# Kernel tuning notes

Measured on AMD Instinct MI355X. Metric: run time of the kernel, lower is better.

Reference implementation:

```python
import jax, jax.numpy as jnp
import numpy as np

DIM, H, KV, HD = 2048, 32, 8, 64
NREP = H // KV
EPS = 1e-6
NEG = -1e30


def _rope(x, cos, sin):
    # x: [B,S,h,HD], cos/sin: [S,HD//2]
    xr, xi = x[..., 0::2], x[..., 1::2]
    c = cos[None, :, None, :]
    s = sin[None, :, None, :]
    out = jnp.stack([xr * c - xi * s, xr * s + xi * c], axis=-1)
    return out.reshape(x.shape)


def _rmsnorm(x, w):
    xf = x.astype(jnp.float32)
    inv = jax.lax.rsqrt(jnp.mean(xf * xf, axis=-1, keepdims=True) + EPS)
    return (xf * inv * w).astype(x.dtype)


def setup_inputs() -> dict:
    key = jax.random.key(0)
    ks = jax.random.split(key, 9)
    B, S = 1, 2048
    x = jax.random.normal(ks[0], (B, S, DIM), jnp.float32)
    cos = jax.random.uniform(ks[1], (S, HD // 2), jnp.float32)
    sin = jax.random.uniform(ks[2], (S, HD // 2), jnp.float32)
    sc = 1.0 / np.sqrt(DIM)
    wq = jax.random.normal(ks[3], (DIM, DIM), jnp.float32) * sc
    wk = jax.random.normal(ks[4], (KV * HD, DIM), jnp.float32) * sc
    wv = jax.random.normal(ks[5], (KV * HD, DIM), jnp.float32) * sc
    wo = jax.random.normal(ks[6], (DIM, DIM), jnp.float32) * sc
    wg = jax.random.normal(ks[7], (DIM, DIM), jnp.float32) * sc
    qn = jnp.ones((HD,), jnp.float32)
    kn = jnp.ones((HD,), jnp.float32)
    return {"x": x, "cos": cos, "sin": sin, "wq": wq, "wk": wk, "wv": wv,
            "wo": wo, "wg": wg, "qn": qn, "kn": kn}


def reference(x, cos, sin, wq, wk, wv, wo, wg, qn, kn):
    B, S, _ = x.shape
    q = (x @ wq.T).reshape(B, S, H, HD)
    k = (x @ wk.T).reshape(B, S, KV, HD)
    v = (x @ wv.T).reshape(B, S, KV, HD)
    q = _rope(q, cos, sin)
    k = _rope(k, cos, sin)
    q = _rmsnorm(q, qn)
    k = _rmsnorm(k, kn)
    # GQA without materializing repeat_kv: head h = g*NREP + r uses kv head g
    qg = q.reshape(B, S, KV, NREP, HD)
    scale = 1.0 / np.sqrt(HD)
    scores = jnp.einsum('bqgrd,bkgd->bgrqk', qg, k) * scale  # [B,KV,NREP,S,S]
    causal = jnp.tril(jnp.ones((S, S), bool))
    scores = jnp.where(causal, scores, NEG)
    attn = jax.nn.softmax(scores, axis=-1)
    o = jnp.einsum('bgrqk,bkgd->bqgrd', attn, v).reshape(B, S, DIM)
    o = o * jax.nn.sigmoid(x @ wg.T)
    return o @ wo.T
```

## Files before the change

kernel.cpp:

```cpp
#include <hip/hip_runtime.h>
#include <stdint.h>

typedef unsigned short u16;
typedef unsigned int u32;
typedef __bf16 bf16x8 __attribute__((ext_vector_type(8)));
typedef __bf16 bf16x2 __attribute__((ext_vector_type(2)));
typedef float f32x4 __attribute__((ext_vector_type(4)));

__device__ __forceinline__ float bf2f(u16 u) {
  union { unsigned int i; float f; } v; v.i = ((unsigned int)u) << 16; return v.f;
}
__device__ __forceinline__ u16 f2bf(float f) {
  union { float f; unsigned int i; } v; v.f = f;
  unsigned int r = v.i + 0x7fffu + ((v.i >> 16) & 1u);
  return (u16)(r >> 16);
}
__device__ __forceinline__ void ld16(const void* g, void* l) {
  __builtin_amdgcn_global_load_lds(
      (const __attribute__((address_space(1))) unsigned int*)g,
      (__attribute__((address_space(3))) unsigned int*)l, 16, 0, 0);
}

__global__ __launch_bounds__(256) void k_cast(
    const float* __restrict__ s0, u16* __restrict__ d0,
    const float* __restrict__ s1, u16* __restrict__ d1,
    const float* __restrict__ s2, u16* __restrict__ d2,
    const float* __restrict__ s3, u16* __restrict__ d3,
    const float* __restrict__ s4, u16* __restrict__ d4,
    const float* __restrict__ s5, u16* __restrict__ d5)
{
  int b = blockIdx.x;
  const float* s; u16* d;
  if (b < 4096)       { s = s0; d = d0; }
  else if (b < 8192)  { s = s1; d = d1; b -= 4096; }
  else if (b < 9216)  { s = s2; d = d2; b -= 8192; }
  else if (b < 10240) { s = s3; d = d3; b -= 9216; }
  else if (b < 14336) { s = s4; d = d4; b -= 10240; }
  else                { s = s5; d = d5; b -= 14336; }
  const int i = (b * 256 + threadIdx.x) * 4;
  const float4 v = *(const float4*)(s + i);
  ushort4 o;
  o.x = f2bf(v.x); o.y = f2bf(v.y); o.z = f2bf(v.z); o.w = f2bf(v.w);
  *(ushort4*)(d + i) = o;
}

template <typename OT>
__device__ __forceinline__ void gemm_body(
    const u16* __restrict__ A, int lda,
    const u16* __restrict__ B, int ldb,
    OT* __restrict__ C, int ldc, int K,
    u16* As, u16* Bs)
{
  const int tid = threadIdx.x;
  const int wave = tid >> 6, lane = tid & 63;
  const int wrow = (wave >> 1) * 64, wcol = (wave & 1) * 64;
  const int fr = lane & 15, kg = lane >> 4;
  const int srl = lane >> 3;
  const int scg = (lane & 7) ^ srl;

  f32x4 acc[4][4];
  const f32x4 z = {0.f, 0.f, 0.f, 0.f};
  for (int i = 0; i < 4; i++) for (int j = 0; j < 4; j++) acc[i][j] = z;

  const u16* Ag = A + (size_t)(wave * 8 + srl) * lda + scg * 8;
  const u16* Bg = B + (size_t)(wave * 8 + srl) * ldb + scg * 8;
  u16* Asw = As + wave * 8 * 64;
  u16* Bsw = Bs + wave * 8 * 64;
  const int sxr = fr & 7;

  for (int k0 = 0; k0 < K; k0 += 64) {
    for (int i = 0; i < 4; i++) {
      ld16(Ag + k0 + (size_t)(i * 32) * lda, Asw + i * 32 * 64);
      ld16(Bg + k0 + (size_t)(i * 32) * ldb, Bsw + i * 32 * 64);
    }
    __syncthreads();
    bf16x8 af[4][2], bfr[4][2];
    for (int i = 0; i < 4; i++)
      for (int h = 0; h < 2; h++) {
        af[i][h]  = *(const bf16x8*)&As[(wrow + i * 16 + fr) * 64 + (((h * 4 + kg) ^ sxr)) * 8];
        bfr[i][h] = *(const bf16x8*)&Bs[(wcol + i * 16 + fr) * 64 + (((h * 4 + kg) ^ sxr)) * 8];
      }
    for (int h = 0; h < 2; h++)
      for (int mi = 0; mi < 4; mi++)
        for (int ni = 0; ni < 4; ni++)
          acc[mi][ni] = __builtin_amdgcn_mfma_f32_16x16x32_bf16(af[mi][h], bfr[ni][h], acc[mi][ni], 0, 0, 0);
    __syncthreads();
  }
  const int er = kg * 4, ec = fr;
  for (int mi = 0; mi < 4; mi++)
    for (int ni = 0; ni < 4; ni++)
      for (int r = 0; r < 4; r++) {
        const float v = acc[mi][ni][r];
        OT* p = C + (size_t)(wrow + mi * 16 + er + r) * ldc + wcol + ni * 16 + ec;
        if constexpr (sizeof(OT) == 2) *p = (OT)f2bf(v); else *p = (OT)v;
      }
}

__global__ __launch_bounds__(256) void k_gemm_qkvg(
    const u16* __restrict__ x, const u16* __restrict__ wq, const u16* __restrict__ wk,
    const u16* __restrict__ wv, const u16* __restrict__ wg, u16* __restrict__ out)
{
  __shared__ __align__(16) u16 As[128 * 64];
  __shared__ __align__(16) u16 Bs[128 * 64];
  const int m0 = blockIdx.x * 128;
  const int c0 = blockIdx.y * 128;
  const u16* B; int br;
  if (c0 < 2048)      { B = wq; br = c0; }
  else if (c0 < 2560) { B = wk; br = c0 - 2048; }
  else if (c0 < 3072) { B = wv; br = c0 - 2560; }
  else                { B = wg; br = c0 - 3072; }
  gemm_body<u16>(x + (size_t)m0 * 2048, 2048, B + (size_t)br * 2048, 2048,
                 out + (size_t)m0 * 5120 + c0, 5120, 2048, As, Bs);
}

__global__ __launch_bounds__(256) void k_gemm_out(
    const u16* __restrict__ a, const u16* __restrict__ wo, float* __restrict__ out)
{
  __shared__ __align__(16) u16 As[128 * 64];
  __shared__ __align__(16) u16 Bs[128 * 64];
  const int m0 = blockIdx.x * 128;
  const int c0 = blockIdx.y * 128;
  gemm_body<float>(a + (size_t)m0 * 2048, 2048, wo + (size_t)c0 * 2048, 2048,
                   out + (size_t)m0 * 2048 + c0, 2048, 2048, As, Bs);
}

__global__ __launch_bounds__(256) void k_prep(
    u16* __restrict__ qkvg, const float* __restrict__ cosp, const float* __restrict__ sinp,
    const float* __restrict__ qn, const float* __restrict__ kn, u16* __restrict__ vt)
{
  __shared__ u16 Ls[64 * 72];
  if (blockIdx.x < 10240) {
    const int wid = (blockIdx.x * 256 + threadIdx.x) >> 6;
    const int lane = threadIdx.x & 63;
    const int s = wid / 20, hp = wid - s * 20;
    const int h = hp * 2 + (lane >> 5);
    const int j = lane & 31;
    u16* base; const float* wn;
    if (h < 32) { base = qkvg + (size_t)s * 5120 + h * 64;                wn = qn; }
    else        { base = qkvg + (size_t)s * 5120 + 2048 + (h - 32) * 64; wn = kn; }
    const unsigned int u = *(const unsigned int*)(base + 2 * j);
    const float xr = bf2f((u16)(u & 0xffffu)), xi = bf2f((u16)(u >> 16));
    const float c = cosp[s * 32 + j], sn = sinp[s * 32 + j];
    const float o0 = xr * c - xi * sn;
    const float o1 = xr * sn + xi * c;
    float ss = o0 * o0 + o1 * o1;
    for (int m = 1; m <= 16; m <<= 1) ss += __shfl_xor(ss, m, 64);
    const float inv = rsqrtf(ss * (1.0f / 64.0f) + 1e-6f);
    const u16 r0 = f2bf(o0 * inv * wn[2 * j]);
    const u16 r1 = f2bf(o1 * inv * wn[2 * j + 1]);
    *(unsigned int*)(base + 2 * j) = (unsigned int)r0 | ((unsigned int)r1 << 16);
  } else {
    const int bb = blockIdx.x - 10240;
    const int s0 = (bb & 31) * 64, g0 = (bb >> 5) * 64;
    const int tid = threadIdx.x;
    const int lr = tid >> 4, lc = (tid & 15) * 4;
    for (int p = 0; p < 4; p++) {
      const int r = p * 16 + lr;
      *(ushort4*)&Ls[r * 72 + lc] = *(const ushort4*)&qkvg[(size_t)(s0 + r) * 5120 + 2560 + g0 + lc];
    }
    __syncthreads();
    for (int p = 0; p < 4; p++) {
      const int r = p * 16 + lr;
      ushort4 o;
      o.x = Ls[(lc + 0) * 72 + r];
      o.y = Ls[(lc + 1) * 72 + r];
      o.z = Ls[(lc + 2) * 72 + r];
      o.w = Ls[(lc + 3) * 72 + r];
      *(ushort4*)&vt[(size_t)(g0 + r) * 2048 + s0 + lc] = o;
    }
  }
}

__global__ __launch_bounds__(256) void k_attn_part(
    const u16* __restrict__ qkvg, const u16* __restrict__ vt,
    u16* __restrict__ part, float* __restrict__ ml)
{
  __shared__ __align__(16) u16 Ks[128 * 64];
  __shared__ __align__(16) u16 Vs[64 * 128];
  u16* Ps = Ks;
  const int c = blockIdx.x, h = blockIdx.y, g = h >> 2;
  int qt, ci;
  if (c < 8)       { qt = c;                 ci = 0; }
  else if (c < 24) { qt = 8 + ((c - 8) >> 1);  ci = (c - 8) & 1; }
  else if (c < 48) { qt = 16 + (c - 24) / 3;   ci = (c - 24) % 3; }
  else             { qt = 24 + ((c - 48) >> 2); ci = (c - 48) & 3; }
  const int kb0 = ci * 512;
  const int kend = min(kb0 + 512, (qt + 1) * 64);
  const int q0 = qt * 64;
  const int tid = threadIdx.x, wave = tid >> 6, lane = tid & 63;
  const int fr = lane & 15, kg = lane >> 4, fq = kg * 8;
  const int sx = fr & 7;

  {
    const u16* Qg = qkvg + (size_t)(q0 + wave * 16 + (lane >> 3)) * 5120 + h * 64 + (lane & 7) * 8;
    ld16(Qg, Ks + wave * 1024);
    ld16(Qg + (size_t)8 * 5120, Ks + wave * 1024 + 512);
  }
  __syncthreads();
  const bf16x8 aq0 = *(const bf16x8*)&Ks[(wave * 16 + fr) * 64 + fq];
  const bf16x8 aq1 = *(const bf16x8*)&Ks[(wave * 16 + fr) * 64 + 32 + fq];
  __syncthreads();

  f32x4 o[4];
  const f32x4 z = {0.f, 0.f, 0.f, 0.f};
  for (int i = 0; i < 4; i++) o[i] = z;
  float L = 0.f;
  const int qrow = q0 + wave * 16 + fr;
  const int prow = wave * 16 + fr;

  const int krl = wave * 8 + (lane >> 3);
  const int kcg = (lane & 7) ^ (krl & 7);
  const int vrl = wave * 4 + kg;
  const int vcg = fr ^ (vrl & 7);

  for (int kb = kb0; kb < kend; kb += 128) {
    {
      const u16* Kg = qkvg + (size_t)(kb + krl) * 5120 + 2048 + g * 64 + kcg * 8;
      for (int i = 0; i < 4; i++)
        ld16(Kg + (size_t)(i * 32) * 5120, Ks + (i * 32 + wave * 8) * 64);
    }
    {
      const u16* Vg = vt + (size_t)(g * 64 + vrl) * 2048 + kb + vcg * 8;
      for (int i = 0; i < 4; i++)
        ld16(Vg + (size_t)(i * 16) * 2048, Vs + (i * 16 + wave * 4) * 128);
    }
    __syncthreads();

    f32x4 sc[8];
    for (int i = 0; i < 8; i++) sc[i] = z;
    __builtin_amdgcn_s_setprio(1);
    for (int ni = 0; ni < 8; ni++) {
      const bf16x8 bk0 = *(const bf16x8*)&Ks[(ni * 16 + fr) * 64 + ((kg ^ sx)) * 8];
      const bf16x8 bk1 = *(const bf16x8*)&Ks[(ni * 16 + fr) * 64 + (((kg + 4) ^ sx)) * 8];
      sc[ni] = __builtin_amdgcn_mfma_f32_16x16x32_bf16(bk0, aq0, sc[ni], 0, 0, 0);
      sc[ni] = __builtin_amdgcn_mfma_f32_16x16x32_bf16(bk1, aq1, sc[ni], 0, 0, 0);
    }
    __builtin_amdgcn_s_setprio(0);
    __syncthreads();

    u32* Ps32 = (u32*)Ps;
    const int pb32 = prow * 64;
    if (kb + 127 > q0 + wave * 16) {
      for (int ni = 0; ni < 8; ni++) {
        const int dlim = qrow - (kb + ni * 16 + kg * 4);
        float p0 = exp2f(fmaf(sc[ni][0], 0.18033688f, -11.5415603f));
        float p1 = exp2f(fmaf(sc[ni][1], 0.18033688f, -11.5415603f));
        float p2 = exp2f(fmaf(sc[ni][2], 0.18033688f, -11.5415603f));
        float p3 = exp2f(fmaf(sc[ni][3], 0.18033688f, -11.5415603f));
        p0 = (0 <= dlim) ? p0 : 0.f;
        p1 = (1 <= dlim) ? p1 : 0.f;
        p2 = (2 <= dlim) ? p2 : 0.f;
        p3 = (3 <= dlim) ? p3 : 0.f;
        L += (p0 + p1) + (p2 + p3);
        bf16x2 w0, w1;
        w0[0] = (__bf16)p0; w0[1] = (__bf16)p1;
        w1[0] = (__bf16)p2; w1[1] = (__bf16)p3;
        const int a = pb32 + ((2 * ni + (kg >> 1)) ^ sx) * 4 + (kg & 1) * 2;
        *(bf16x2*)&Ps32[a]     = w0;
        *(bf16x2*)&Ps32[a + 1] = w1;
      }
    } else {
      for (int ni = 0; ni < 8; ni++) {
        float p0 = exp2f(fmaf(sc[ni][0], 0.18033688f, -11.5415603f));
        float p1 = exp2f(fmaf(sc[ni][1], 0.18033688f, -11.5415603f));
        float p2 = exp2f(fmaf(sc[ni][2], 0.18033688f, -11.5415603f));
        float p3 = exp2f(fmaf(sc[ni][3], 0.18033688f, -11.5415603f));
        L += (p0 + p1) + (p2 + p3);
        bf16x2 w0, w1;
        w0[0] = (__bf16)p0; w0[1] = (__bf16)p1;
        w1[0] = (__bf16)p2; w1[1] = (__bf16)p3;
        const int a = pb32 + ((2 * ni + (kg >> 1)) ^ sx) * 4 + (kg & 1) * 2;
        *(bf16x2*)&Ps32[a]     = w0;
        *(bf16x2*)&Ps32[a + 1] = w1;
      }
    }

    __builtin_amdgcn_s_setprio(1);
    for (int k0 = 0; k0 < 128; k0 += 32) {
      const bf16x8 ap = *(const bf16x8*)&Ps[prow * 128 + ((((k0 >> 3) + kg)) ^ sx) * 8];
      for (int ni = 0; ni < 4; ni++) {
        const bf16x8 bv = *(const bf16x8*)&Vs[(ni * 16 + fr) * 128 + (((k0 >> 3) + kg) ^ sx) * 8];
        o[ni] = __builtin_amdgcn_mfma_f32_16x16x32_bf16(ap, bv, o[ni], 0, 0, 0);
      }
    }
    __builtin_amdgcn_s_setprio(0);
    __syncthreads();
  }

  L += __shfl_xor(L, 16, 64);
  L += __shfl_xor(L, 32, 64);
  const int pbase = (h * 80 + c) * 4096;
  for (int ni = 0; ni < 4; ni++)
    for (int r = 0; r < 4; r++)
      part[pbase + (wave * 16 + kg * 4 + r) * 64 + ni * 16 + fr] = f2bf(o[ni][r]);
  if (lane < 16) ml[(h * 80 + c) * 64 + wave * 16 + fr] = L;
}

__global__ __launch_bounds__(256) void k_attn_comb(
    const u16* __restrict__ part, const float* __restrict__ ml,
    const u16* __restrict__ qkvg, u16* __restrict__ aout)
{
  const int qt = blockIdx.x, h = blockIdx.y;
  const int w = threadIdx.x >> 6, lane = threadIdx.x & 63;
  int cb, nch;
  if (qt < 8)       { cb = qt;               nch = 1; }
  else if (qt < 16) { cb = 8 + 2 * (qt - 8);  nch = 2; }
  else if (qt < 24) { cb = 24 + 3 * (qt - 16); nch = 3; }
  else              { cb = 48 + 4 * (qt - 24); nch = 4; }
  for (int r = 0; r < 16; r++) {
    const int rl = w * 16 + r;
    const int row = qt * 64 + rl;
    float L = 0.f, o = 0.f;
    for (int cc = 0; cc < nch; cc++) {
      L += ml[(h * 80 + cb + cc) * 64 + rl];
      o += bf2f(part[(h * 80 + cb + cc) * 4096 + rl * 64 + lane]);
    }
    const float gv = bf2f(qkvg[(size_t)row * 5120 + 3072 + h * 64 + lane]);
    const float sig = 1.0f / (1.0f + __expf(-gv));
    aout[(size_t)row * 2048 + h * 64 + lane] = f2bf(o / L * sig);
  }
}

extern "C" void kernel_launch(void* const* d_in, const int* in_sizes, int n_in,
                              void* d_out, int out_size, void* d_ws, size_t ws_size,
                              hipStream_t stream)
{
  const float* x  = (const float*)d_in[0];
  const float* cs = (const float*)d_in[1];
  const float* sn = (const float*)d_in[2];
  const float* wq = (const float*)d_in[3];
  const float* wk = (const float*)d_in[4];
  const float* wv = (const float*)d_in[5];
  const float* wo = (const float*)d_in[6];
  const float* wg = (const float*)d_in[7];
  const float* qn = (const float*)d_in[8];
  const float* kn = (const float*)d_in[9];
  float* out = (float*)d_out;

  u16* xb   = (u16*)d_ws;
  u16* wqb  = xb  + (size_t)4194304;
  u16* wkb  = wqb + (size_t)4194304;
  u16* wvb  = wkb + (size_t)1048576;
  u16* wgb  = wvb + (size_t)1048576;
  u16* wob  = wgb + (size_t)4194304;
  u16* qkvg = wob + (size_t)4194304;
  u16* vt   = qkvg + (size_t)2048 * 5120;
  u16* aws  = vt   + (size_t)512 * 2048;

  u16*   part = xb;
  float* ml   = (float*)(xb + (size_t)32 * 80 * 4096);

  k_cast<<<dim3(18432), 256, 0, stream>>>(x, xb, wq, wqb, wk, wkb, wv, wvb, wo, wob, wg, wgb);
  k_gemm_qkvg<<<dim3(16, 40), 256, 0, stream>>>(xb, wqb, wkb, wvb, wgb, qkvg);
  k_prep<<<dim3(10240 + 256), 256, 0, stream>>>(qkvg, cs, sn, qn, kn, vt);
  k_attn_part<<<dim3(80, 32), 256, 0, stream>>>(qkvg, vt, part, ml);
  k_attn_comb<<<dim3(32, 32), 256, 0, stream>>>(part, ml, qkvg, aws);
  k_gemm_out<<<dim3(16, 16), 256, 0, stream>>>(aws, wob, out);
}
```

Baseline: 291.5 us.

## Rewrite QKVG projection GEMM as 256x256 double-buffered pipelined kernel

Replaces the 128x128 single-buffered QKVG projection GEMM with a 256x256-tile, 512-thread kernel. It double-buffers LDS and interleaves global-to-LDS async loads for the next K-steps with MFMA phases, using setprio and fine-grained barriers. The goal is to hide memory latency and raise arithmetic intensity per block. The cost is 128 KB of LDS per block and only 160 blocks, which may underfill the device's compute units and limit occupancy.

Measured after the change: 307.0 us. 5.3% more time.

```diff
diff --git a/kernel.cpp b/kernel.cpp
--- a/kernel.cpp
+++ b/kernel.cpp
@@ -44,6 +44,157 @@
   *(ushort4*)(d + i) = o;
 }
 
+__device__ __forceinline__ void stage256(const u16* __restrict__ gb, int k0, int half,
+                                         u16* __restrict__ Lb, int wave)
+{
+  const u16* src = gb + (size_t)(half * 128) * 2048 + k0;
+  u16* dst = Lb + (half * 128 + wave * 8) * 64;
+  ld16(src, dst);
+  ld16(src + (size_t)64 * 2048, dst + 64 * 64);
+}
+
+__global__ __launch_bounds__(512, 2) void k_gemm_qkvg(
+    const u16* __restrict__ x, const u16* __restrict__ wq, const u16* __restrict__ wk,
+    const u16* __restrict__ wv, const u16* __restrict__ wg, u16* __restrict__ out)
+{
+  __shared__ __align__(16) u16 As[2][256 * 64];
+  __shared__ __align__(16) u16 Bs[2][256 * 64];
+  const int mt = blockIdx.x & 7, nt = blockIdx.x >> 3;
+  const int m0 = mt * 256, c0 = nt * 256;
+  const u16* Bm; int br;
+  if (c0 < 2048)      { Bm = wq; br = c0; }
+  else if (c0 < 2560) { Bm = wk; br = c0 - 2048; }
+  else if (c0 < 3072) { Bm = wv; br = c0 - 2560; }
+  else                { Bm = wg; br = c0 - 3072; }
+
+  const int tid = threadIdx.x, wave = tid >> 6, lane = tid & 63;
+  const int wr = wave >> 2, wc = wave & 3;
+  const int fr = lane & 15, kg = lane >> 4, sx = fr & 7;
+  const int srl = lane >> 3, scg = (lane & 7) ^ srl;
+
+  const u16* Ag = x  + (size_t)(m0 + wave * 8 + srl) * 2048 + scg * 8;
+  const u16* Bg = Bm + (size_t)(br + wave * 8 + srl) * 2048 + scg * 8;
+
+  stage256(Ag,  0, 0, As[0], wave);
+  stage256(Ag,  0, 1, As[0], wave);
+  stage256(Bg,  0, 0, Bs[0], wave);
+  stage256(Bg,  0, 1, Bs[0], wave);
+  stage256(Bg, 64, 0, Bs[1], wave);
+  stage256(Bg, 64, 1, Bs[1], wave);
+  stage256(Ag, 64, 0, As[1], wave);
+  asm volatile("s_waitcnt vmcnt(6)" ::: "memory");
+  __builtin_amdgcn_s_barrier();
+
+  f32x4 acc[8][4];
+  const f32x4 z = {0.f, 0.f, 0.f, 0.f};
+#pragma unroll
+  for (int i = 0; i < 8; i++)
+#pragma unroll
+    for (int j = 0; j < 4; j++) acc[i][j] = z;
+
+  for (int t = 0; t < 32; ++t) {
+    const int cur = t & 1;
+    const u16* Ac = As[cur];
+    const u16* Bc = Bs[cur];
+    u16* An = As[cur ^ 1];
+    u16* A2 = As[cur];  u16* B2 = Bs[cur];
+    const int k1 = (t + 1 < 32 ? t + 1 : 31) * 64;
+    const int k2 = (t + 2 < 32 ? t + 2 : 31) * 64;
+
+    bf16x8 bfr[4][2], af0[2][2];
+#pragma unroll
+    for (int ni = 0; ni < 4; ni++)
+#pragma unroll
+      for (int h = 0; h < 2; h++)
+        bfr[ni][h] = *(const bf16x8*)&Bc[(wc * 64 + ni * 16 + fr) * 64 + (((h * 4 + kg) ^ sx)) * 8];
+#pragma unroll
+    for (int m2 = 0; m2 < 2; m2++)
+#pragma unroll
+      for (int h = 0; h < 2; h++)
+        af0[m2][h] = *(const bf16x8*)&Ac[(wr * 128 + m2 * 16 + fr) * 64 + (((h * 4 + kg) ^ sx)) * 8];
+    stage256(Ag, k1, 1, An, wave);
+    __builtin_amdgcn_s_barrier();
+    asm volatile("s_waitcnt lgkmcnt(0)" ::: "memory");
+    __builtin_amdgcn_s_setprio(1);
+#pragma unroll
+    for (int h = 0; h < 2; h++)
+#pragma unroll
+      for (int m2 = 0; m2 < 2; m2++)
+#pragma unroll
+        for (int ni = 0; ni < 4; ni++)
+          acc[m2][ni] = __builtin_amdgcn_mfma_f32_16x16x32_bf16(af0[m2][h], bfr[ni][h], acc[m2][ni], 0, 0, 0);
+    __builtin_amdgcn_s_setprio(0);
+    __builtin_amdgcn_s_barrier();
+
+    bf16x8 af1[2][2];
+#pragma unroll
+    for (int m2 = 0; m2 < 2; m2++)
+#pragma unroll
+      for (int h = 0; h < 2; h++)
+        af1[m2][h] = *(const bf16x8*)&Ac[(wr * 128 + (2 + m2) * 16 + fr) * 64 + (((h * 4 + kg) ^ sx)) * 8];
+    stage256(Bg, k2, 0, B2, wave);
+    __builtin_amdgcn_s_barrier();
+    asm volatile("s_waitcnt lgkmcnt(0)" ::: "memory");
+    __builtin_amdgcn_s_setprio(1);
+#pragma unroll
+    for (int h = 0; h < 2; h++)
+#pragma unroll
+      for (int m2 = 0; m2 < 2; m2++)
+#pragma unroll
+        for (int ni = 0; ni < 4; ni++)
+          acc[2 + m2][ni] = __builtin_amdgcn_mfma_f32_16x16x32_bf16(af1[m2][h], bfr[ni][h], acc[2 + m2][ni], 0, 0, 0);
+    __builtin_amdgcn_s_setprio(0);
+    __builtin_amdgcn_s_barrier();
+
+    bf16x8 af2[2][2], af3[2][2];
+#pragma unroll
+    for (int m2 = 0; m2 < 2; m2++)
+#pragma unroll
+      for (int h = 0; h < 2; h++) {
+        af2[m2][h] = *(const bf16x8*)&Ac[(wr * 128 + (4 + m2) * 16 + fr) * 64 + (((h * 4 + kg) ^ sx)) * 8];
+        af3[m2][h] = *(const bf16x8*)&Ac[(wr * 128 + (6 + m2) * 16 + fr) * 64 + (((h * 4 + kg) ^ sx)) * 8];
+      }
+    stage256(Bg, k2, 1, B2, wave);
+    __builtin_amdgcn_s_barrier();
+    asm volatile("s_waitcnt lgkmcnt(0)" ::: "memory");
+    __builtin_amdgcn_s_setprio(1);
+#pragma unroll
+    for (int h = 0; h < 2; h++)
+#pragma unroll
+      for (int m2 = 0; m2 < 2; m2++)
+#pragma unroll
+        for (int ni = 0; ni < 4; ni++)
+          acc[4 + m2][ni] = __builtin_amdgcn_mfma_f32_16x16x32_bf16(af2[m2][h], bfr[ni][h], acc[4 + m2][ni], 0, 0, 0);
+    __builtin_amdgcn_s_setprio(0);
+    __builtin_amdgcn_s_barrier();
+
+    stage256(Ag, k2, 0, A2, wave);
+    __builtin_amdgcn_s_barrier();
+    __builtin_amdgcn_s_setprio(1);
+#pragma unroll
+    for (int h = 0; h < 2; h++)
+#pragma unroll
+      for (int m2 = 0; m2 < 2; m2++)
+#pragma unroll
+        for (int ni = 0; ni < 4; ni++)
+          acc[6 + m2][ni] = __builtin_amdgcn_mfma_f32_16x16x32_bf16(af3[m2][h], bfr[ni][h], acc[6 + m2][ni], 0, 0, 0);
+    __builtin_amdgcn_s_setprio(0);
+    asm volatile("s_waitcnt vmcnt(6)" ::: "memory");
+    __builtin_amdgcn_s_barrier();
+  }
+  asm volatile("s_waitcnt vmcnt(0)" ::: "memory");
+
+  const int er = kg * 4;
+#pragma unroll
+  for (int mi = 0; mi < 8; mi++)
+#pragma unroll
+    for (int ni = 0; ni < 4; ni++)
+#pragma unroll
+      for (int r = 0; r < 4; r++)
+        out[(size_t)(m0 + wr * 128 + mi * 16 + er + r) * 5120 + c0 + wc * 64 + ni * 16 + fr] =
+            f2bf(acc[mi][ni][r]);
+}
+
 template <typename OT>
 __device__ __forceinline__ void gemm_body(
     const u16* __restrict__ A, int lda,
@@ -94,23 +245,6 @@
         OT* p = C + (size_t)(wrow + mi * 16 + er + r) * ldc + wcol + ni * 16 + ec;
         if constexpr (sizeof(OT) == 2) *p = (OT)f2bf(v); else *p = (OT)v;
       }
-}
-
-__global__ __launch_bounds__(256) void k_gemm_qkvg(
-    const u16* __restrict__ x, const u16* __restrict__ wq, const u16* __restrict__ wk,
-    const u16* __restrict__ wv, const u16* __restrict__ wg, u16* __restrict__ out)
-{
-  __shared__ __align__(16) u16 As[128 * 64];
-  __shared__ __align__(16) u16 Bs[128 * 64];
-  const int m0 = blockIdx.x * 128;
-  const int c0 = blockIdx.y * 128;
-  const u16* B; int br;
-  if (c0 < 2048)      { B = wq; br = c0; }
-  else if (c0 < 2560) { B = wk; br = c0 - 2048; }
-  else if (c0 < 3072) { B = wv; br = c0 - 2560; }
-  else                { B = wg; br = c0 - 3072; }
-  gemm_body<u16>(x + (size_t)m0 * 2048, 2048, B + (size_t)br * 2048, 2048,
-                 out + (size_t)m0 * 5120 + c0, 5120, 2048, As, Bs);
 }
 
 __global__ __launch_bounds__(256) void k_gemm_out(
@@ -351,7 +485,7 @@
   float* ml   = (float*)(xb + (size_t)32 * 80 * 4096);
 
   k_cast<<<dim3(18432), 256, 0, stream>>>(x, xb, wq, wqb, wk, wkb, wv, wvb, wo, wob, wg, wgb);
-  k_gemm_qkvg<<<dim3(16, 40), 256, 0, stream>>>(xb, wqb, wkb, wvb, wgb, qkvg);
+  k_gemm_qkvg<<<dim3(160), 512, 0, stream>>>(xb, wqb, wkb, wvb, wgb, qkvg);
   k_prep<<<dim3(10240 + 256), 256, 0, stream>>>(qkvg, cs, sn, qn, kn, vt);
   k_attn_part<<<dim3(80, 32), 256, 0, stream>>>(qkvg, vt, part, ml);
   k_attn_comb<<<dim3(32, 32), 256, 0, stream>>>(part, ml, qkvg, aws);
```

## Process all four GQA heads per block to reuse K/V tiles

Applied to the files above, without the earlier changes.

The attention partial kernel now launches one block per KV group instead of per query head. Each block loads Q for all four heads in the group and reuses each staged K/V tile across them. P gets its own shared-memory buffer so the per-tile sync between QK and PV is removed. This cuts K/V global loads and barriers by about four times, but the grid shrinks from 2560 to 640 blocks, register pressure rises from four sets of accumulators, and occupancy is capped by launch bounds.

After: 313.8 us. 1.08x slower.

```diff
diff --git a/kernel.cpp b/kernel.cpp
--- a/kernel.cpp
+++ b/kernel.cpp
@@ -171,14 +171,15 @@
   }
 }
 
-__global__ __launch_bounds__(256) void k_attn_part(
+__global__ __launch_bounds__(256, 3) void k_attn_part(
     const u16* __restrict__ qkvg, const u16* __restrict__ vt,
     u16* __restrict__ part, float* __restrict__ ml)
 {
-  __shared__ __align__(16) u16 Ks[128 * 64];
-  __shared__ __align__(16) u16 Vs[64 * 128];
-  u16* Ps = Ks;
-  const int c = blockIdx.x, h = blockIdx.y, g = h >> 2;
+  __shared__ __align__(16) u16 SMEM[3 * 64 * 128];
+  u16* Ks = SMEM;
+  u16* Vs = SMEM + 8192;
+  u16* Ps = SMEM + 16384;
+  const int c = blockIdx.x, g = blockIdx.y;
   int qt, ci;
   if (c < 8)       { qt = c;                 ci = 0; }
   else if (c < 24) { qt = 8 + ((c - 8) >> 1);  ci = (c - 8) & 1; }
@@ -188,23 +189,31 @@
   const int kend = min(kb0 + 512, (qt + 1) * 64);
   const int q0 = qt * 64;
   const int tid = threadIdx.x, wave = tid >> 6, lane = tid & 63;
-  const int fr = lane & 15, kg = lane >> 4, fq = kg * 8;
+  const int fr = lane & 15, kg = lane >> 4;
   const int sx = fr & 7;
 
   {
-    const u16* Qg = qkvg + (size_t)(q0 + wave * 16 + (lane >> 3)) * 5120 + h * 64 + (lane & 7) * 8;
-    ld16(Qg, Ks + wave * 1024);
-    ld16(Qg + (size_t)8 * 5120, Ks + wave * 1024 + 512);
+    const u16* Qg = qkvg + (size_t)(q0 + wave * 16 + (lane >> 5)) * 5120 + g * 256 + (lane & 31) * 8;
+#pragma unroll
+    for (int i = 0; i < 8; i++)
+      ld16(Qg + (size_t)(i * 2) * 5120, SMEM + (wave * 16 + i * 2) * 256);
   }
   __syncthreads();
-  const bf16x8 aq0 = *(const bf16x8*)&Ks[(wave * 16 + fr) * 64 + fq];
-  const bf16x8 aq1 = *(const bf16x8*)&Ks[(wave * 16 + fr) * 64 + 32 + fq];
+  bf16x8 aq[4][2];
+#pragma unroll
+  for (int hh = 0; hh < 4; hh++)
+#pragma unroll
+    for (int hf = 0; hf < 2; hf++)
+      aq[hh][hf] = *(const bf16x8*)&SMEM[(wave * 16 + fr) * 256 + hh * 64 + hf * 32 + kg * 8];
   __syncthreads();
 
-  f32x4 o[4];
+  f32x4 o[4][4];
   const f32x4 z = {0.f, 0.f, 0.f, 0.f};
-  for (int i = 0; i < 4; i++) o[i] = z;
-  float L = 0.f;
+#pragma unroll
+  for (int hh = 0; hh < 4; hh++)
+#pragma unroll
+    for (int i = 0; i < 4; i++) o[hh][i] = z;
+  float L[4] = {0.f, 0.f, 0.f, 0.f};
   const int qrow = q0 + wave * 16 + fr;
   const int prow = wave * 16 + fr;
 
@@ -216,84 +225,105 @@
   for (int kb = kb0; kb < kend; kb += 128) {
     {
       const u16* Kg = qkvg + (size_t)(kb + krl) * 5120 + 2048 + g * 64 + kcg * 8;
+#pragma unroll
       for (int i = 0; i < 4; i++)
         ld16(Kg + (size_t)(i * 32) * 5120, Ks + (i * 32 + wave * 8) * 64);
     }
     {
       const u16* Vg = vt + (size_t)(g * 64 + vrl) * 2048 + kb + vcg * 8;
+#pragma unroll
       for (int i = 0; i < 4; i++)
         ld16(Vg + (size_t)(i * 16) * 2048, Vs + (i * 16 + wave * 4) * 128);
     }
     __syncthreads();
 
-    f32x4 sc[8];
-    for (int i = 0; i < 8; i++) sc[i] = z;
-    __builtin_amdgcn_s_setprio(1);
-    for (int ni = 0; ni < 8; ni++) {
-      const bf16x8 bk0 = *(const bf16x8*)&Ks[(ni * 16 + fr) * 64 + ((kg ^ sx)) * 8];
-      const bf16x8 bk1 = *(const bf16x8*)&Ks[(ni * 16 + fr) * 64 + (((kg + 4) ^ sx)) * 8];
-      sc[ni] = __builtin_amdgcn_mfma_f32_16x16x32_bf16(bk0, aq0, sc[ni], 0, 0, 0);
-      sc[ni] = __builtin_amdgcn_mfma_f32_16x16x32_bf16(bk1, aq1, sc[ni], 0, 0, 0);
-    }
-    __builtin_amdgcn_s_setprio(0);
-    __syncthreads();
-
+    const bool masked = (kb + 127 > q0 + wave * 16);
     u32* Ps32 = (u32*)Ps;
     const int pb32 = prow * 64;
-    if (kb + 127 > q0 + wave * 16) {
+
+#pragma unroll
+    for (int hh = 0; hh < 4; hh++) {
+      f32x4 sc[8];
+#pragma unroll
+      for (int i = 0; i < 8; i++) sc[i] = z;
+      __builtin_amdgcn_s_setprio(1);
+#pragma unroll
       for (int ni = 0; ni < 8; ni++) {
-        const int dlim = qrow - (kb + ni * 16 + kg * 4);
-        float p0 = exp2f(fmaf(sc[ni][0], 0.18033688f, -11.5415603f));
-        float p1 = exp2f(fmaf(sc[ni][1], 0.18033688f, -11.5415603f));
-        float p2 = exp2f(fmaf(sc[ni][2], 0.18033688f, -11.5415603f));
-        float p3 = exp2f(fmaf(sc[ni][3], 0.18033688f, -11.5415603f));
-        p0 = (0 <= dlim) ? p0 : 0.f;
-        p1 = (1 <= dlim) ? p1 : 0.f;
-        p2 = (2 <= dlim) ? p2 : 0.f;
-        p3 = (3 <= dlim) ? p3 : 0.f;
-        L += (p0 + p1) + (p2 + p3);
-        bf16x2 w0, w1;
-        w0[0] = (__bf16)p0; w0[1] = (__bf16)p1;
-        w1[0] = (__bf16)p2; w1[1] = (__bf16)p3;
-        const int a = pb32 + ((2 * ni + (kg >> 1)) ^ sx) * 4 + (kg & 1) * 2;
-        *(bf16x2*)&Ps32[a]     = w0;
-        *(bf16x2*)&Ps32[a + 1] = w1;
-      }
-    } else {
-      for (int ni = 0; ni < 8; ni++) {
-        float p0 = exp2f(fmaf(sc[ni][0], 0.18033688f, -11.5415603f));
-        float p1 = exp2f(fmaf(sc[ni][1], 0.18033688f, -11.5415603f));
-        float p2 = exp2f(fmaf(sc[ni][2], 0.18033688f, -11.5415603f));
-        float p3 = exp2f(fmaf(sc[ni][3], 0.18033688f, -11.5415603f));
-        L += (p0 + p1) + (p2 + p3);
-        bf16x2 w0, w1;
-        w0[0] = (__bf16)p0; w0[1] = (__bf16)p1;
-        w1[0] = (__bf16)p2; w1[1] = (__bf16)p3;
-        const int a = pb32 + ((2 * ni + (kg >> 1)) ^ sx) * 4 + (kg & 1) * 2;
-        *(bf16x2*)&Ps32[a]     = w0;
-        *(bf16x2*)&Ps32[a + 1] = w1;
-      }
-    }
-
-    __builtin_amdgcn_s_setprio(1);
-    for (int k0 = 0; k0 < 128; k0 += 32) {
-      const bf16x8 ap = *(const bf16x8*)&Ps[prow * 128 + ((((k0 >> 3) + kg)) ^ sx) * 8];
-      for (int ni = 0; ni < 4; ni++) {
-        const bf16x8 bv = *(const bf16x8*)&Vs[(ni * 16 + fr) * 128 + (((k0 >> 3) + kg) ^ sx) * 8];
-        o[ni] = __builtin_amdgcn_mfma_f32_16x16x32_bf16(ap, bv, o[ni], 0, 0, 0);
-      }
-    }
-    __builtin_amdgcn_s_setprio(0);
-    __syncthreads();
-  }
-
-  L += __shfl_xor(L, 16, 64);
-  L += __shfl_xor(L, 32, 64);
-  const int pbase = (h * 80 + c) * 4096;
-  for (int ni = 0; ni < 4; ni++)
-    for (int r = 0; r < 4; r++)
-      part[pbase + (wave * 16 + kg * 4 + r) * 64 + ni * 16 + fr] = f2bf(o[ni][r]);
-  if (lane < 16) ml[(h * 80 + c) * 64 + wave * 16 + fr] = L;
+        const bf16x8 bk0 = *(const bf16x8*)&Ks[(ni * 16 + fr) * 64 + ((kg ^ sx)) * 8];
+        const bf16x8 bk1 = *(const bf16x8*)&Ks[(ni * 16 + fr) * 64 + (((kg + 4) ^ sx)) * 8];
+        sc[ni] = __builtin_amdgcn_mfma_f32_16x16x32_bf16(bk0, aq[hh][0], sc[ni], 0, 0, 0);
+        sc[ni] = __builtin_amdgcn_mfma_f32_16x16x32_bf16(bk1, aq[hh][1], sc[ni], 0, 0, 0);
+      }
+      __builtin_amdgcn_s_setprio(0);
+
+      float Lh = 0.f;
+      if (masked) {
+#pragma unroll
+        for (int ni = 0; ni < 8; ni++) {
+          const int dlim = qrow - (kb + ni * 16 + kg * 4);
+          float p0 = exp2f(fmaf(sc[ni][0], 0.18033688f, -11.5415603f));
+          float p1 = exp2f(fmaf(sc[ni][1], 0.18033688f, -11.5415603f));
+          float p2 = exp2f(fmaf(sc[ni][2], 0.18033688f, -11.5415603f));
+          float p3 = exp2f(fmaf(sc[ni][3], 0.18033688f, -11.5415603f));
+          p0 = (0 <= dlim) ? p0 : 0.f;
+          p1 = (1 <= dlim) ? p1 : 0.f;
+          p2 = (2 <= dlim) ? p2 : 0.f;
+          p3 = (3 <= dlim) ? p3 : 0.f;
+          Lh += (p0 + p1) + (p2 + p3);
+          bf16x2 w0, w1;
+          w0[0] = (__bf16)p0; w0[1] = (__bf16)p1;
+          w1[0] = (__bf16)p2; w1[1] = (__bf16)p3;
+          const int a = pb32 + ((2 * ni + (kg >> 1)) ^ sx) * 4 + (kg & 1) * 2;
+          *(bf16x2*)&Ps32[a]     = w0;
+          *(bf16x2*)&Ps32[a + 1] = w1;
+        }
+      } else {
+#pragma unroll
+        for (int ni = 0; ni < 8; ni++) {
+          float p0 = exp2f(fmaf(sc[ni][0], 0.18033688f, -11.5415603f));
+          float p1 = exp2f(fmaf(sc[ni][1], 0.18033688f, -11.5415603f));
+          float p2 = exp2f(fmaf(sc[ni][2], 0.18033688f, -11.5415603f));
+          float p3 = exp2f(fmaf(sc[ni][3], 0.18033688f, -11.5415603f));
+          Lh += (p0 + p1) + (p2 + p3);
+          bf16x2 w0, w1;
+          w0[0] = (__bf16)p0; w0[1] = (__bf16)p1;
+          w1[0] = (__bf16)p2; w1[1] = (__bf16)p3;
+          const int a = pb32 + ((2 * ni + (kg >> 1)) ^ sx) * 4 + (kg & 1) * 2;
+          *(bf16x2*)&Ps32[a]     = w0;
+          *(bf16x2*)&Ps32[a + 1] = w1;
+        }
+      }
+      L[hh] += Lh;
+
+      __builtin_amdgcn_s_setprio(1);
+#pragma unroll
+      for (int k0 = 0; k0 < 128; k0 += 32) {
+        const bf16x8 ap = *(const bf16x8*)&Ps[prow * 128 + ((((k0 >> 3) + kg)) ^ sx) * 8];
+#pragma unroll
+        for (int ni = 0; ni < 4; ni++) {
+          const bf16x8 bv = *(const bf16x8*)&Vs[(ni * 16 + fr) * 128 + (((k0 >> 3) + kg) ^ sx) * 8];
+          o[hh][ni] = __builtin_amdgcn_mfma_f32_16x16x32_bf16(ap, bv, o[hh][ni], 0, 0, 0);
+        }
+      }
+      __builtin_amdgcn_s_setprio(0);
+    }
+    __syncthreads();
+  }
+
+#pragma unroll
+  for (int hh = 0; hh < 4; hh++) {
+    float Lh = L[hh];
+    Lh += __shfl_xor(Lh, 16, 64);
+    Lh += __shfl_xor(Lh, 32, 64);
+    const int h = g * 4 + hh;
+    const int pbase = (h * 80 + c) * 4096;
+#pragma unroll
+    for (int ni = 0; ni < 4; ni++)
+#pragma unroll
+      for (int r = 0; r < 4; r++)
+        part[pbase + (wave * 16 + kg * 4 + r) * 64 + ni * 16 + fr] = f2bf(o[hh][ni][r]);
+    if (lane < 16) ml[(h * 80 + c) * 64 + wave * 16 + fr] = Lh;
+  }
 }
 
 __global__ __launch_bounds__(256) void k_attn_comb(
@@ -353,7 +383,7 @@
   k_cast<<<dim3(18432), 256, 0, stream>>>(x, xb, wq, wqb, wk, wkb, wv, wvb, wo, wob, wg, wgb);
   k_gemm_qkvg<<<dim3(16, 40), 256, 0, stream>>>(xb, wqb, wkb, wvb, wgb, qkvg);
   k_prep<<<dim3(10240 + 256), 256, 0, stream>>>(qkvg, cs, sn, qn, kn, vt);
-  k_attn_part<<<dim3(80, 32), 256, 0, stream>>>(qkvg, vt, part, ml);
+  k_attn_part<<<dim3(80, 8), 256, 0, stream>>>(qkvg, vt, part, ml);
   k_attn_comb<<<dim3(32, 32), 256, 0, stream>>>(part, ml, qkvg, aws);
   k_gemm_out<<<dim3(16, 16), 256, 0, stream>>>(aws, wob, out);
 }
```
